# Optimization experiments

Hardware: AMD Instinct MI355X
Metric: run time of the kernel (lower is better)

## Reference

```python
import jax, jax.numpy as jnp
import numpy as np

LARGE_NUMBER = 1.0e8
C_CLIP = 10.0
TEMP = 1.0
N_HISTORY = 3


def setup_inputs() -> dict:
    key = jax.random.key(0)
    ks = jax.random.split(key, 6)
    B, S, H, Q = 128, 256, 512, 360
    inputs = jax.random.normal(ks[0], (B, S, H), dtype=jnp.float32)
    Wc = jax.random.normal(ks[1], (H, H), dtype=jnp.float32) / np.sqrt(H)
    bc = jnp.zeros((H,), dtype=jnp.float32)
    Wq = jax.random.normal(ks[2], (N_HISTORY, H, Q), dtype=jnp.float32) / np.sqrt(H)
    w_q = jax.random.normal(ks[3], (Q, H), dtype=jnp.float32) / np.sqrt(Q)
    v = jax.random.normal(ks[4], (H,), dtype=jnp.float32) / np.sqrt(H)
    return {"inputs": inputs, "Wc": Wc, "bc": bc, "Wq": Wq, "w_q": w_q, "v": v}


def reference(inputs, Wc, bc, Wq, w_q, v):
    B, S, H = inputs.shape
    # 1x1 Conv1d over channels == per-position linear
    enc = jnp.einsum('bsh,ho->bso', inputs, Wc) + bc  # [B,S,H]
    batch_idx = jnp.arange(B)

    def step(carry, _):
        mask, prev, key = carry  # mask [B,S], prev [n_hist,B,H]
        key, sk = jax.random.split(key)
        query = jax.nn.relu(jnp.einsum('kbh,khq->bq', prev, Wq))        # [B,Q]
        eq = query @ w_q                                                  # [B,H]
        scores = jnp.einsum('h,bsh->bs', v, jnp.tanh(enc + eq[:, None, :]))
        scores = C_CLIP * jnp.tanh(scores / TEMP)
        masked = jnp.clip(scores - LARGE_NUMBER * mask, -LARGE_NUMBER, LARGE_NUMBER)
        idx = jax.random.categorical(sk, masked)                          # [B]
        logp = jax.nn.log_softmax(masked, axis=-1)
        lp = jnp.take_along_axis(logp, idx[:, None], axis=1)[:, 0]        # [B]
        ent = -jnp.sum(jnp.exp(logp) * logp, axis=-1)                     # [B]
        mask = mask.at[batch_idx, idx].set(1.0)
        action = inputs[batch_idx, idx]                                   # [B,H]
        prev = jnp.concatenate([prev[1:], action[None]], axis=0)
        return (mask, prev, key), (idx, lp, ent)

    mask0 = jnp.zeros((B, S), dtype=inputs.dtype)
    prev0 = jnp.zeros((N_HISTORY, B, H), dtype=inputs.dtype)
    key0 = jax.random.key(1)
    _, (idxs, lps, ents) = jax.lax.scan(step, (mask0, prev0, key0), None, length=S)
    tour = jnp.concatenate([idxs.T, idxs.T[:, :1]], axis=1)  # [B, S+1], close loop
    log_probs = jnp.sum(lps)
    entropies = jnp.sum(ents)
    return tour, log_probs, entropies
```

## Files before the change

### kernel.cpp

```cpp
#include <hip/hip_runtime.h>
#include <hip/hip_fp16.h>
#include <stdint.h>

#define BB 128
#define SS 256
#define HH 512
#define QQ 360
#define QP 384
#define QP2 192
#define HF 256

struct TF2 { uint32_t a, b; };

__host__ __device__ constexpr uint32_t rotl32(uint32_t x, int d) {
  return (x << d) | (x >> (32 - d));
}

__host__ __device__ constexpr TF2 threefry(uint32_t k0, uint32_t k1,
                                           uint32_t x0, uint32_t x1) {
  uint32_t ks[3] = {k0, k1, k0 ^ k1 ^ 0x1BD11BDAu};
  x0 += ks[0]; x1 += ks[1];
  const int R0[4] = {13, 15, 26, 6};
  const int R1[4] = {17, 29, 16, 24};
  for (int g = 0; g < 5; ++g) {
    const int* r = (g & 1) ? R1 : R0;
    for (int i = 0; i < 4; ++i) { x0 += x1; x1 = rotl32(x1, r[i]); x1 ^= x0; }
    x0 += ks[(g + 1) % 3];
    x1 += ks[(g + 2) % 3] + (uint32_t)(g + 1);
  }
  return TF2{x0, x1};
}

struct KeyTab { uint32_t sk[256][2]; };
constexpr KeyTab make_keys() {
  KeyTab K{};
  uint32_t k0 = 0u, k1 = 1u;
  for (int t = 0; t < 256; ++t) {
    TF2 nk = threefry(k0, k1, 0u, 0u);
    TF2 sk = threefry(k0, k1, 0u, 1u);
    K.sk[t][0] = sk.a; K.sk[t][1] = sk.b;
    k0 = nk.a; k1 = nk.b;
  }
  return K;
}
__constant__ KeyTab c_keys = make_keys();

__device__ __forceinline__ float frcp(float x) {
#if __has_builtin(__builtin_amdgcn_rcpf)
  return __builtin_amdgcn_rcpf(x);
#else
  return 1.0f / x;
#endif
}

#if __has_builtin(__builtin_amdgcn_exp2f)
  #define EXP2F(x) __builtin_amdgcn_exp2f(x)
  #define CC 2.8853900817779268f
#else
  #define EXP2F(x) __expf(x)
  #define CC 2.0f
#endif

#define ENC_SCALE 21.0f
#define ENC_INV (CC / ENC_SCALE)

__device__ __forceinline__ float fast_tanh(float x) {
  float e = __expf(2.0f * x);
  return 1.0f - 2.0f * frcp(e + 1.0f);
}

typedef _Float16 f16x2 __attribute__((ext_vector_type(2)));

__global__ __launch_bounds__(256) void k_enc(const float* __restrict__ inputs,
                                             const float* __restrict__ Wc,
                                             const float* __restrict__ bc,
                                             int8_t* __restrict__ enc8) {
  const int ht = blockIdx.x;
  const int b  = blockIdx.y;
  const int tid = threadIdx.x;
  const int ts = tid & 63, th = tid >> 6;
  __shared__ float Xs[32 * 260];
  __shared__ float Ws[32 * 64];
  float acc[16][4];
#pragma unroll
  for (int i = 0; i < 16; ++i)
#pragma unroll
    for (int j = 0; j < 4; ++j) acc[i][j] = 0.f;

  const float* Arow = inputs + ((size_t)b * SS + tid) * HH;
  for (int kk = 0; kk < HH; kk += 32) {
    const float4* ip = (const float4*)(Arow + kk);
#pragma unroll
    for (int e = 0; e < 8; ++e) {
      float4 w = ip[e];
      Xs[(e * 4 + 0) * 260 + tid] = w.x;
      Xs[(e * 4 + 1) * 260 + tid] = w.y;
      Xs[(e * 4 + 2) * 260 + tid] = w.z;
      Xs[(e * 4 + 3) * 260 + tid] = w.w;
    }
    {
      int kw = tid >> 3, hw = (tid & 7) * 8;
      const float4* wp = (const float4*)(Wc + (size_t)(kk + kw) * HH + ht * 64 + hw);
      float4 w0 = wp[0], w1 = wp[1];
      float* d = Ws + kw * 64 + hw;
      ((float4*)d)[0] = w0; ((float4*)d)[1] = w1;
    }
    __syncthreads();
#pragma unroll 8
    for (int k = 0; k < 32; ++k) {
      float xr[4];
#pragma unroll
      for (int j = 0; j < 4; ++j) xr[j] = Xs[k * 260 + ts + 64 * j];
      const float4* wr4 = (const float4*)(Ws + k * 64 + th * 16);
#pragma unroll
      for (int i4 = 0; i4 < 4; ++i4) {
        float4 w = wr4[i4];
        float wv[4] = {w.x, w.y, w.z, w.w};
#pragma unroll
        for (int c = 0; c < 4; ++c)
#pragma unroll
          for (int j = 0; j < 4; ++j) acc[i4 * 4 + c][j] += wv[c] * xr[j];
      }
    }
    __syncthreads();
  }
#pragma unroll
  for (int i = 0; i < 16; ++i) {
    int h = ht * 64 + th * 16 + i;
    float bcv = bc[h];
    int8_t* orow = enc8 + (size_t)b * (HH * SS) + (size_t)h * SS + ts;
#pragma unroll
    for (int j = 0; j < 4; ++j) {
      float q = rintf(fminf(fmaxf((acc[i][j] + bcv) * ENC_SCALE, -127.f), 127.f));
      orow[64 * j] = (int8_t)(int)q;
    }
  }
}

__global__ __launch_bounds__(256) void k_G(const float* __restrict__ inputs,
                                           const float* __restrict__ Wq,
                                           __half* __restrict__ G) {
  const int qt = blockIdx.x;
  const int b  = blockIdx.y;
  const int k  = blockIdx.z;
  const int tid = threadIdx.x;
  const int ql = tid & 63, tj = tid >> 6;
  __shared__ float Xs[32 * 260];
  __shared__ float Ws[32 * 64];
  float acc[64];
#pragma unroll
  for (int j = 0; j < 64; ++j) acc[j] = 0.f;
  const int q = qt * 64 + ql;
  const float* Arow = inputs + ((size_t)b * SS + tid) * HH;
  const float* Wqk = Wq + (size_t)k * HH * QQ;
  for (int kk = 0; kk < HH; kk += 32) {
    const float4* ip = (const float4*)(Arow + kk);
#pragma unroll
    for (int e = 0; e < 8; ++e) {
      float4 w = ip[e];
      Xs[(e * 4 + 0) * 260 + tid] = w.x;
      Xs[(e * 4 + 1) * 260 + tid] = w.y;
      Xs[(e * 4 + 2) * 260 + tid] = w.z;
      Xs[(e * 4 + 3) * 260 + tid] = w.w;
    }
    {
      int hh = tid >> 3, qw = (tid & 7) * 8;
      const float* src = Wqk + (size_t)(kk + hh) * QQ;
      float* d = Ws + hh * 64 + qw;
#pragma unroll
      for (int e = 0; e < 8; ++e) {
        int qg = qt * 64 + qw + e;
        d[e] = (qg < QQ) ? src[qg] : 0.f;
      }
    }
    __syncthreads();
#pragma unroll 4
    for (int k2 = 0; k2 < 32; ++k2) {
      float wr = Ws[k2 * 64 + ql];
      const float4* xp = (const float4*)(Xs + k2 * 260 + tj * 64);
#pragma unroll
      for (int j4 = 0; j4 < 16; ++j4) {
        float4 x = xp[j4];
        acc[j4 * 4 + 0] += wr * x.x;
        acc[j4 * 4 + 1] += wr * x.y;
        acc[j4 * 4 + 2] += wr * x.z;
        acc[j4 * 4 + 3] += wr * x.w;
      }
    }
    __syncthreads();
  }
  if (q < QQ) {
#pragma unroll
    for (int j = 0; j < 64; ++j) {
      size_t jg = (size_t)b * SS + (tj * 64 + j);
      G[(jg * 3 + k) * QQ + q] = __float2half(acc[j]);
    }
  }
}

__global__ __launch_bounds__(1024) void k_w2(const float* __restrict__ w_q,
                                             __half2* __restrict__ W2) {
  int t = blockIdx.x * 1024 + threadIdx.x;
  if (t < QP2 * HH) {
    int qp = t / HH, h = t % HH;
    float a = (2 * qp < QQ) ? w_q[(size_t)(2 * qp) * HH + h] : 0.f;
    float b = (2 * qp + 1 < QQ) ? w_q[(size_t)(2 * qp + 1) * HH + h] : 0.f;
    W2[t] = __floats2half2_rn(a, b);
  }
}

__global__ __launch_bounds__(1024, 4) void k_scan(
    const __half2* __restrict__ W2, const float* __restrict__ v,
    const int8_t* __restrict__ enc8, const __half* __restrict__ G,
    float* __restrict__ xm, uint32_t* __restrict__ xflag,
    float* __restrict__ out, double* __restrict__ lpb, double* __restrict__ entb) {
  const int bid = blockIdx.x;
  const int b = bid & 127;
  const int half = bid >> 7;
  const int tid = (int)threadIdx.x;
  const int lane = tid & 63;
  const int wid = tid >> 6;
  const int q_sub = lane >> 2;
  const int hq2 = lane & 3;
  const int hl = lane >> 5;
  const int sl = lane & 31;
  const int sbase = sl * 8;
  const int s4 = tid >> 2;
  const int rq = tid & 3;

  __shared__ uint2 enc_lds[HF * 32];
  __shared__ float2 evq[HF];
  __shared__ __half2 q2_s[QP2];
  __shared__ float q12_s[QP];
  __shared__ float part[16][260];
  __shared__ float m_s[SS];
  __shared__ float mask_s[SS];
  __shared__ float4 wred[16];
  __shared__ int hist[3];
  __shared__ float Vtot_s;

  const int hbase = half * HF;

  if (tid < HF) evq[tid] = make_float2(0.f, -2.0f * v[hbase + tid]);
  if (tid < SS) mask_s[tid] = 0.f;
  if (tid < QP) q12_s[tid] = 0.f;
  if (tid < QP2) q2_s[tid] = __floats2half2_rn(0.f, 0.f);
  if (tid < 3) hist[tid] = -1;
  if (tid < 64) {
    float s = 0.f;
#pragma unroll
    for (int j = 0; j < 8; ++j) s += v[tid + 64 * j];
#pragma unroll
    for (int off = 32; off; off >>= 1) s += __shfl_xor(s, off);
    if (tid == 0) Vtot_s = s;
  }
  {
    const uint4* src4 = (const uint4*)(enc8 + (size_t)b * (HH * SS) + (size_t)hbase * SS);
    uint4* dst4 = (uint4*)enc_lds;
#pragma unroll
    for (int it = 0; it < 4; ++it)
      dst4[it * 1024 + tid] = src4[it * 1024 + tid];
  }
  __syncthreads();
  const float Vtot = Vtot_s;

  const __half* Gb = G + (size_t)b * SS * 3 * QQ;
  const __half2* wp2 = W2 + (size_t)(q_sub * 12) * HH + hbase + wid * 16 + hq2 * 4;
  const uint2* encL = enc_lds + (size_t)(wid * 16 + hl) * 32 + sl;
  float* xm_my = xm + (size_t)(b * 2 + half) * 512;
  const float* xm_pr = xm + (size_t)(b * 2 + (1 - half)) * 512;
  uint32_t* flag_my = xflag + (size_t)bid * 16;
  uint32_t* flag_pr = xflag + (size_t)(bid ^ 128) * 16;

  double lp_acc = 0.0, ent_acc = 0.0;
  int first_idx = 0;

  for (int t = 0; t < SS; ++t) {
    const int p0 = hist[1], p1 = hist[2];
    uint2 g0raw = make_uint2(0, 0), g1raw = make_uint2(0, 0);
    const bool pf = (tid < 90);
    if (pf) {
      if (p0 >= 0) g0raw = *(const uint2*)(Gb + ((size_t)p0 * 3 + 0) * QQ + 4 * tid);
      if (p1 >= 0) g1raw = *(const uint2*)(Gb + ((size_t)p1 * 3 + 1) * QQ + 4 * tid);
    }

    float gum, maskv;
    {
      TF2 o = threefry(c_keys.sk[t][0], c_keys.sk[t][1], 0u, (uint32_t)(b * SS + s4));
      float fb = __uint_as_float((o.b >> 9) | 0x3f800000u) - 1.0f;
      fb = fmaxf(fb, 1.0e-12f);
      gum = -__logf(-__logf(fb));
      maskv = mask_s[s4];
    }

    {
      float a[4];
#pragma unroll
      for (int j = 0; j < 4; ++j) a[j] = 0.f;
      const __half2* qsp = q2_s + q_sub * 12;
#pragma unroll 4
      for (int i = 0; i < 12; ++i) {
        uint4 raw = *(const uint4*)(wp2 + (size_t)i * HH);
        __half2 qv = qsp[i];
#if __has_builtin(__builtin_amdgcn_fdot2)
        f16x2 qf = *(f16x2*)&qv;
        a[0] = __builtin_amdgcn_fdot2(qf, *(f16x2*)&raw.x, a[0], false);
        a[1] = __builtin_amdgcn_fdot2(qf, *(f16x2*)&raw.y, a[1], false);
        a[2] = __builtin_amdgcn_fdot2(qf, *(f16x2*)&raw.z, a[2], false);
        a[3] = __builtin_amdgcn_fdot2(qf, *(f16x2*)&raw.w, a[3], false);
#else
        float2 qf = __half22float2(qv);
        float2 w0 = __half22float2(*(const __half2*)&raw.x);
        float2 w1 = __half22float2(*(const __half2*)&raw.y);
        float2 w2 = __half22float2(*(const __half2*)&raw.z);
        float2 w3 = __half22float2(*(const __half2*)&raw.w);
        a[0] = fmaf(qf.x, w0.x, fmaf(qf.y, w0.y, a[0]));
        a[1] = fmaf(qf.x, w1.x, fmaf(qf.y, w1.y, a[1]));
        a[2] = fmaf(qf.x, w2.x, fmaf(qf.y, w2.y, a[2]));
        a[3] = fmaf(qf.x, w3.x, fmaf(qf.y, w3.y, a[3]));
#endif
      }
#pragma unroll
      for (int off = 4; off <= 32; off <<= 1)
#pragma unroll
        for (int j = 0; j < 4; ++j) a[j] += __shfl_xor(a[j], off);
      if (lane < 4) {
        int h0 = wid * 16 + lane * 4;
#pragma unroll
        for (int j = 0; j < 4; ++j) evq[h0 + j].x = CC * a[j];
      }
    }

    {
      float acc[8];
#pragma unroll
      for (int j = 0; j < 8; ++j) acc[j] = 0.f;
#pragma unroll
      for (int i = 0; i < 8; ++i) {
        float2 ev = evq[wid * 16 + 2 * i + hl];
        const float eqC = ev.x, mv = ev.y;
        uint2 w = encL[(size_t)(2 * i) * 32];
        const uint32_t w0 = w.x, w1 = w.y;
#pragma unroll
        for (int k = 0; k < 4; ++k) {
          {
            float f = (float)(int)(int8_t)(w0 >> (8 * k));
            float e = EXP2F(fmaf(f, ENC_INV, eqC));
            acc[k] = fmaf(mv, frcp(e + 1.0f), acc[k]);
          }
          {
            float f = (float)(int)(int8_t)(w1 >> (8 * k));
            float e = EXP2F(fmaf(f, ENC_INV, eqC));
            acc[4 + k] = fmaf(mv, frcp(e + 1.0f), acc[4 + k]);
          }
        }
      }
#pragma unroll
      for (int j = 0; j < 8; ++j) acc[j] += __shfl_xor(acc[j], 32);
      if (hl == 0) {
        *(float4*)&part[wid][sbase]     = make_float4(acc[0], acc[1], acc[2], acc[3]);
        *(float4*)&part[wid][sbase + 4] = make_float4(acc[4], acc[5], acc[6], acc[7]);
      }
    }

    if (pf) {
      float2 f0a = __half22float2(*(const __half2*)&g0raw.x);
      float2 f0b = __half22float2(*(const __half2*)&g0raw.y);
      float2 f1a = __half22float2(*(const __half2*)&g1raw.x);
      float2 f1b = __half22float2(*(const __half2*)&g1raw.y);
      float4 qv;
      qv.x = f0a.x + f1a.x; qv.y = f0a.y + f1a.y;
      qv.z = f0b.x + f1b.x; qv.w = f0b.y + f1b.y;
      *(float4*)&q12_s[4 * tid] = qv;
    }
    __syncthreads();

    float own;
    {
      own  = part[rq * 4 + 0][s4];
      own += part[rq * 4 + 1][s4];
      own += part[rq * 4 + 2][s4];
      own += part[rq * 4 + 3][s4];
      own += __shfl_xor(own, 1);
      own += __shfl_xor(own, 2);
      if (rq == 0)
        __hip_atomic_store(&xm_my[(t & 1) * 256 + s4], own,
                           __ATOMIC_RELAXED, __HIP_MEMORY_SCOPE_AGENT);
    }
    __syncthreads();
    if (tid == 0) {
      __hip_atomic_store(flag_my, (uint32_t)(t + 1),
                         __ATOMIC_RELEASE, __HIP_MEMORY_SCOPE_AGENT);
      while (__hip_atomic_load(flag_pr, __ATOMIC_RELAXED,
                               __HIP_MEMORY_SCOPE_AGENT) < (uint32_t)(t + 1))
        __builtin_amdgcn_s_sleep(1);
    }
    __syncthreads();

    {
      float peer = __hip_atomic_load(&xm_pr[(t & 1) * 256 + s4],
                                     __ATOMIC_RELAXED, __HIP_MEMORY_SCOPE_AGENT);
      float sc = Vtot + (own + peer);
      float logit = 10.0f * fast_tanh(sc);
      float m = (maskv != 0.f) ? -1.0e8f : logit;
      if (rq == 0) m_s[s4] = m;
      float z = m + gum;
      float e = __expf(m);
      float em = e * m;
      int si = s4;
#pragma unroll
      for (int off = 4; off <= 32; off <<= 1) {
        float zo = __shfl_xor(z, off);
        int io = __shfl_xor(si, off);
        if (zo > z || (zo == z && io < si)) { z = zo; si = io; }
        e += __shfl_xor(e, off);
        em += __shfl_xor(em, off);
      }
      if (lane == 0) wred[wid] = make_float4(z, __int_as_float(si), e, em);
    }
    __syncthreads();

    {
      float4 r0 = wred[0];
      float z = r0.x; int si = __float_as_int(r0.y);
      float se = r0.z, sem = r0.w;
#pragma unroll
      for (int r = 1; r < 16; ++r) {
        float4 rv = wred[r];
        int io = __float_as_int(rv.y);
        if (rv.x > z || (rv.x == z && io < si)) { z = rv.x; si = io; }
        se += rv.z; sem += rv.w;
      }
      const int idx = si;
      if (pf) {
        uint2 g2 = *(const uint2*)(Gb + ((size_t)idx * 3 + 2) * QQ + 4 * tid);
        float2 f2a = __half22float2(*(const __half2*)&g2.x);
        float2 f2b = __half22float2(*(const __half2*)&g2.y);
        float4 q12v = *(const float4*)&q12_s[4 * tid];
        float4 qn;
        qn.x = fmaxf(q12v.x + f2a.x, 0.f);
        qn.y = fmaxf(q12v.y + f2a.y, 0.f);
        qn.z = fmaxf(q12v.z + f2b.x, 0.f);
        qn.w = fmaxf(q12v.w + f2b.y, 0.f);
        q2_s[2 * tid]     = __floats2half2_rn(qn.x, qn.y);
        q2_s[2 * tid + 1] = __floats2half2_rn(qn.z, qn.w);
      }
      if (tid == 0) {
        float lse = __logf(se);
        float mi = m_s[idx];
        lp_acc += (double)(mi - lse);
        ent_acc += (double)(lse - sem / se);
        if (half == 0) out[b * 257 + t] = (float)idx;
        mask_s[idx] = 1.0f;
        hist[0] = hist[1]; hist[1] = hist[2]; hist[2] = idx;
        if (t == 0) first_idx = idx;
      }
    }
    __syncthreads();
  }

  if (tid == 0 && half == 0) {
    out[b * 257 + 256] = (float)first_idx;
    lpb[b] = lp_acc;
    entb[b] = ent_acc;
  }
}

__global__ void k_final(const double* __restrict__ lpb,
                        const double* __restrict__ entb, float* __restrict__ out) {
  if (threadIdx.x == 0) {
    double a = 0.0, c = 0.0;
    for (int i = 0; i < BB; ++i) { a += lpb[i]; c += entb[i]; }
    out[BB * 257 + 0] = (float)a;
    out[BB * 257 + 1] = (float)c;
  }
}

extern "C" void kernel_launch(void* const* d_in, const int* in_sizes, int n_in,
                              void* d_out, int out_size, void* d_ws, size_t ws_size,
                              hipStream_t stream) {
  const float* inputs = (const float*)d_in[0];
  const float* Wc  = (const float*)d_in[1];
  const float* bc  = (const float*)d_in[2];
  const float* Wq  = (const float*)d_in[3];
  const float* w_q = (const float*)d_in[4];
  const float* v   = (const float*)d_in[5];
  float* out = (float*)d_out;

  char* ws = (char*)d_ws;
  const size_t encBytes = (size_t)BB * HH * SS;
  const size_t gBytes   = (size_t)3 * BB * SS * QQ * 2;
  const size_t w2Bytes  = (size_t)QP2 * HH * 4;
  int8_t* enc8 = (int8_t*)ws;
  __half* G   = (__half*)(ws + encBytes);
  __half2* W2 = (__half2*)(ws + encBytes + gBytes);
  size_t xoff = (encBytes + gBytes + w2Bytes + 1023) & ~(size_t)1023;
  float* xm = (float*)(ws + xoff);
  uint32_t* xflag = (uint32_t*)(ws + xoff + 512 * 1024);
  double* lpb = (double*)(ws + xoff + 512 * 1024 + 16384);
  double* entb = lpb + BB;

  dim3 gA1(8, BB);
  k_enc<<<gA1, 256, 0, stream>>>(inputs, Wc, bc, enc8);
  dim3 gA2(6, BB, 3);
  k_G<<<gA2, 256, 0, stream>>>(inputs, Wq, G);
  k_w2<<<(QP2 * HH + 1023) / 1024, 1024, 0, stream>>>(w_q, W2);
  hipMemsetAsync(xflag, 0, 16384, stream);

  void* args[] = {(void*)&W2, (void*)&v, (void*)&enc8, (void*)&G,
                  (void*)&xm, (void*)&xflag, (void*)&out, (void*)&lpb, (void*)&entb};
  hipError_t ce = hipLaunchCooperativeKernel((const void*)k_scan, dim3(256), dim3(1024),
                                             args, 0, stream);
  if (ce != hipSuccess) {
    k_scan<<<256, 1024, 0, stream>>>(W2, v, enc8, G, xm, xflag, out, lpb, entb);
  }
  k_final<<<1, 64, 0, stream>>>(lpb, entb, out);
}
```

Measured before the change: 3.851 ms.

## Replace flag handshake with per-element sequence-tagged 64-bit exchange

```diff
diff --git a/kernel.cpp b/kernel.cpp
--- a/kernel.cpp
+++ b/kernel.cpp
@@ -212,7 +212,7 @@
 __global__ __launch_bounds__(1024, 4) void k_scan(
     const __half2* __restrict__ W2, const float* __restrict__ v,
     const int8_t* __restrict__ enc8, const __half* __restrict__ G,
-    float* __restrict__ xm, uint32_t* __restrict__ xflag,
+    uint64_t* __restrict__ xm,
     float* __restrict__ out, double* __restrict__ lpb, double* __restrict__ entb) {
   const int bid = blockIdx.x;
   const int b = bid & 127;
@@ -267,10 +267,8 @@
   const __half* Gb = G + (size_t)b * SS * 3 * QQ;
   const __half2* wp2 = W2 + (size_t)(q_sub * 12) * HH + hbase + wid * 16 + hq2 * 4;
   const uint2* encL = enc_lds + (size_t)(wid * 16 + hl) * 32 + sl;
-  float* xm_my = xm + (size_t)(b * 2 + half) * 512;
-  const float* xm_pr = xm + (size_t)(b * 2 + (1 - half)) * 512;
-  uint32_t* flag_my = xflag + (size_t)bid * 16;
-  uint32_t* flag_pr = xflag + (size_t)(bid ^ 128) * 16;
+  uint64_t* xm_my = xm + (size_t)(b * 2 + half) * 512;
+  const uint64_t* xm_pr = xm + (size_t)(b * 2 + (1 - half)) * 512;
 
   double lp_acc = 0.0, ent_acc = 0.0;
   int first_idx = 0;
@@ -278,19 +276,10 @@
   for (int t = 0; t < SS; ++t) {
     const int p0 = hist[1], p1 = hist[2];
     uint2 g0raw = make_uint2(0, 0), g1raw = make_uint2(0, 0);
-    const bool pf = (tid < 90);
+    const bool pf = (tid < 96);
     if (pf) {
       if (p0 >= 0) g0raw = *(const uint2*)(Gb + ((size_t)p0 * 3 + 0) * QQ + 4 * tid);
       if (p1 >= 0) g1raw = *(const uint2*)(Gb + ((size_t)p1 * 3 + 1) * QQ + 4 * tid);
-    }
-
-    float gum, maskv;
-    {
-      TF2 o = threefry(c_keys.sk[t][0], c_keys.sk[t][1], 0u, (uint32_t)(b * SS + s4));
-      float fb = __uint_as_float((o.b >> 9) | 0x3f800000u) - 1.0f;
-      fb = fmaxf(fb, 1.0e-12f);
-      gum = -__logf(-__logf(fb));
-      maskv = mask_s[s4];
     }
 
     {
@@ -383,23 +372,31 @@
       own += part[rq * 4 + 3][s4];
       own += __shfl_xor(own, 1);
       own += __shfl_xor(own, 2);
-      if (rq == 0)
-        __hip_atomic_store(&xm_my[(t & 1) * 256 + s4], own,
+      if (rq == 0) {
+        uint64_t pk = ((uint64_t)__float_as_uint(own) << 32) | (uint32_t)(t + 1);
+        __hip_atomic_store(&xm_my[(t & 1) * 256 + s4], pk,
                            __ATOMIC_RELAXED, __HIP_MEMORY_SCOPE_AGENT);
-    }
-    __syncthreads();
-    if (tid == 0) {
-      __hip_atomic_store(flag_my, (uint32_t)(t + 1),
-                         __ATOMIC_RELEASE, __HIP_MEMORY_SCOPE_AGENT);
-      while (__hip_atomic_load(flag_pr, __ATOMIC_RELAXED,
-                               __HIP_MEMORY_SCOPE_AGENT) < (uint32_t)(t + 1))
+      }
+    }
+
+    float gum, maskv;
+    {
+      TF2 o = threefry(c_keys.sk[t][0], c_keys.sk[t][1], 0u, (uint32_t)(b * SS + s4));
+      float fb = __uint_as_float((o.b >> 9) | 0x3f800000u) - 1.0f;
+      fb = fmaxf(fb, 1.0e-12f);
+      gum = -__logf(-__logf(fb));
+      maskv = mask_s[s4];
+    }
+
+    {
+      uint64_t pv = __hip_atomic_load(&xm_pr[(t & 1) * 256 + s4],
+                                      __ATOMIC_RELAXED, __HIP_MEMORY_SCOPE_AGENT);
+      while ((uint32_t)pv != (uint32_t)(t + 1)) {
         __builtin_amdgcn_s_sleep(1);
-    }
-    __syncthreads();
-
-    {
-      float peer = __hip_atomic_load(&xm_pr[(t & 1) * 256 + s4],
-                                     __ATOMIC_RELAXED, __HIP_MEMORY_SCOPE_AGENT);
+        pv = __hip_atomic_load(&xm_pr[(t & 1) * 256 + s4],
+                               __ATOMIC_RELAXED, __HIP_MEMORY_SCOPE_AGENT);
+      }
+      float peer = __uint_as_float((uint32_t)(pv >> 32));
       float sc = Vtot + (own + peer);
       float logit = 10.0f * fast_tanh(sc);
       float m = (maskv != 0.f) ? -1.0e8f : logit;
@@ -432,7 +429,7 @@
         se += rv.z; sem += rv.w;
       }
       const int idx = si;
-      if (pf) {
+      if (tid < 90) {
         uint2 g2 = *(const uint2*)(Gb + ((size_t)idx * 3 + 2) * QQ + 4 * tid);
         float2 f2a = __half22float2(*(const __half2*)&g2.x);
         float2 f2b = __half22float2(*(const __half2*)&g2.y);
@@ -495,9 +492,8 @@
   __half* G   = (__half*)(ws + encBytes);
   __half2* W2 = (__half2*)(ws + encBytes + gBytes);
   size_t xoff = (encBytes + gBytes + w2Bytes + 1023) & ~(size_t)1023;
-  float* xm = (float*)(ws + xoff);
-  uint32_t* xflag = (uint32_t*)(ws + xoff + 512 * 1024);
-  double* lpb = (double*)(ws + xoff + 512 * 1024 + 16384);
+  uint64_t* xm = (uint64_t*)(ws + xoff);
+  double* lpb = (double*)(ws + xoff + 1024 * 1024);
   double* entb = lpb + BB;
 
   dim3 gA1(8, BB);
@@ -505,14 +501,14 @@
   dim3 gA2(6, BB, 3);
   k_G<<<gA2, 256, 0, stream>>>(inputs, Wq, G);
   k_w2<<<(QP2 * HH + 1023) / 1024, 1024, 0, stream>>>(w_q, W2);
-  hipMemsetAsync(xflag, 0, 16384, stream);
+  hipMemsetAsync(xm, 0, 1024 * 1024, stream);
 
   void* args[] = {(void*)&W2, (void*)&v, (void*)&enc8, (void*)&G,
-                  (void*)&xm, (void*)&xflag, (void*)&out, (void*)&lpb, (void*)&entb};
+                  (void*)&xm, (void*)&out, (void*)&lpb, (void*)&entb};
   hipError_t ce = hipLaunchCooperativeKernel((const void*)k_scan, dim3(256), dim3(1024),
                                              args, 0, stream);
   if (ce != hipSuccess) {
-    k_scan<<<256, 1024, 0, stream>>>(W2, v, enc8, G, xm, xflag, out, lpb, entb);
+    k_scan<<<256, 1024, 0, stream>>>(W2, v, enc8, G, xm, out, lpb, entb);
   }
   k_final<<<1, 64, 0, stream>>>(lpb, entb, out);
 }
```

After: 3.635 ms. -5.6%, faster.
